# Kernel optimization log

Hardware: AMD Instinct MI355X
Metric: run time of the kernel (lower is better)

The kernel has to match this reference:

```python
import jax, jax.numpy as jnp
import numpy as np

B, N_PER, F_IN, HID, DEG = 64, 1024, 64, 128, 16
N = B * N_PER
E = N * DEG

def _ceil_k(k):
    return -((-4 * k) // 5)  # ceil(0.8 * k), static python int

def setup_inputs():
    key = jax.random.key(0)
    ks = jax.random.split(key, 16)
    x = jax.random.normal(ks[0], (N, F_IN), jnp.float32)
    # edges are intra-graph: local endpoints in [0, N_PER) offset by graph id
    loc = jax.random.randint(ks[1], (2, E), 0, N_PER, jnp.int32)
    gid = jnp.repeat(jnp.arange(B, dtype=jnp.int32), E // B)
    edge_index = loc + gid[None, :] * N_PER
    batch = jnp.repeat(jnp.arange(B, dtype=jnp.int32), N_PER)
    def lin(k, fi, fo):
        s = 1.0 / float(np.sqrt(fi))
        return jax.random.uniform(k, (fi, fo), jnp.float32, -s, s)
    inp = dict(x=x, edge_index=edge_index, batch=batch)
    inp["Wr1"] = lin(ks[2], F_IN, HID); inp["Wn1"] = lin(ks[3], F_IN, HID); inp["b1"] = jnp.zeros((HID,), jnp.float32)
    inp["Wr2"] = lin(ks[4], HID, HID); inp["Wn2"] = lin(ks[5], HID, HID); inp["b2"] = jnp.zeros((HID,), jnp.float32)
    inp["Wr3"] = lin(ks[6], HID, HID); inp["Wn3"] = lin(ks[7], HID, HID); inp["b3"] = jnp.zeros((HID,), jnp.float32)
    inp["p1"] = jax.random.normal(ks[8], (HID,), jnp.float32)
    inp["p2"] = jax.random.normal(ks[9], (HID,), jnp.float32)
    inp["p3"] = jax.random.normal(ks[10], (HID,), jnp.float32)
    inp["l1w"] = lin(ks[11], 2 * HID, HID); inp["l1b"] = jnp.zeros((HID,), jnp.float32)
    inp["l2w"] = lin(ks[12], HID, 2); inp["l2b"] = jnp.zeros((2,), jnp.float32)
    return inp

def _graph_conv(x, src, dst, emask, Wr, Wn, b, n_nodes):
    # x'_i = W1 x_i + sum_{j->i} W2 x_j + b ; masked edges contribute 0
    msg = x[src] * emask[:, None]                                  # [E, H]
    agg = jax.ops.segment_sum(msg, dst, num_segments=n_nodes)     # [N, H]
    return x @ Wr + agg @ Wn + b

def _topk_pool(x, src, dst, emask, p, k_prev):
    # PyG TopKPooling: score = x.p/||p||, keep ceil(0.8*n) per graph,
    # x_out = x[perm] * tanh(score[perm]); relabel+filter edges
    k_new = _ceil_k(k_prev)
    s = (x @ p) / jnp.linalg.norm(p)                               # [B*k_prev]
    vals, idx = jax.lax.top_k(s.reshape(B, k_prev), k_new)        # [B, k_new]
    perm = (idx + jnp.arange(B, dtype=idx.dtype)[:, None] * k_prev).reshape(-1)
    x_new = x[perm] * jnp.tanh(vals.reshape(-1))[:, None]
    inv = jnp.full((B * k_prev,), -1, jnp.int32).at[perm].set(jnp.arange(B * k_new, dtype=jnp.int32))
    ns, nd = inv[src], inv[dst]
    valid = emask * ((ns >= 0) & (nd >= 0)).astype(x.dtype)
    return x_new, jnp.maximum(ns, 0), jnp.maximum(nd, 0), valid, k_new

def _readout(x, k):
    b = jnp.repeat(jnp.arange(B, dtype=jnp.int32), k)
    gmax = jax.ops.segment_max(x, b, num_segments=B)
    gmean = jax.ops.segment_sum(x, b, num_segments=B) / k
    return jnp.concatenate([gmax, gmean], axis=1)                  # [B, 2H]

def reference(x, edge_index, batch, Wr1, Wn1, b1, Wr2, Wn2, b2, Wr3, Wn3, b3, p1, p2, p3, l1w, l1b, l2w, l2b):
    src, dst = edge_index[0], edge_index[1]
    emask = jnp.ones((E,), x.dtype)
    k = N_PER
    convs = [(Wr1, Wn1, b1), (Wr2, Wn2, b2), (Wr3, Wn3, b3)]
    pools = [p1, p2, p3]
    xs = []
    for (Wr, Wn, bb), p in zip(convs, pools):
        x = jax.nn.relu(_graph_conv(x, src, dst, emask, Wr, Wn, bb, B * k))
        x, src, dst, emask, k = _topk_pool(x, src, dst, emask, p, k)
        xs.append(_readout(x, k))
    h = xs[0] + xs[1] + xs[2]
    h = jax.nn.relu(h @ l1w + l1b)
    # F.dropout(p=0.5) skipped: eval-mode reference
    h = jax.nn.relu(h @ l2w + l2b)
    return jax.nn.log_softmax(h, axis=-1)
```

## Files before the change

### kernel.cpp

```cpp
#include <hip/hip_runtime.h>
#include <hip/hip_bf16.h>
#include <math.h>

#define NN   65536
#define NPER 1024
#define NE   1048576
#define NB   64
#define EPG  16384

typedef __attribute__((ext_vector_type(8))) short short8;
typedef __attribute__((ext_vector_type(4))) float f32x4;


__global__ __launch_bounds__(1024) void csr_kernel(const int* __restrict__ ei,
      int* __restrict__ off, int* __restrict__ adj){
  __shared__ int hist[1024];
  __shared__ int wsum[16];
  const int g = ((int)blockIdx.x & 7)*8 + ((int)blockIdx.x >> 3);
  const int t = threadIdx.x;
  const int ebase = g*EPG, nbase = g*NPER;
  hist[t] = 0;
  __syncthreads();
  int srcs[16], dls[16];
  #pragma unroll
  for (int i = 0; i < 16; ++i){
    int e = ebase + t + i*1024;
    srcs[i] = ei[e];
    dls[i]  = ei[NE + e] - nbase;
    atomicAdd(&hist[dls[i]], 1);
  }
  __syncthreads();
  int v = hist[t];
  int lane = t & 63, wid = t >> 6;
  int s = v;
  #pragma unroll
  for (int d = 1; d < 64; d <<= 1){
    int src = (lane >= d) ? (lane - d) : lane;
    int u = __shfl(s, src);
    if (lane >= d) s += u;
  }
  if (lane == 63) wsum[wid] = s;
  __syncthreads();
  if (wid == 0){
    int ws = (lane < 16) ? wsum[lane] : 0;
    #pragma unroll
    for (int d = 1; d < 16; d <<= 1){
      int src = (lane >= d) ? (lane - d) : lane;
      int u = __shfl(ws, src);
      if (lane >= d) ws += u;
    }
    if (lane < 16) wsum[lane] = ws;
  }
  __syncthreads();
  int base = (wid > 0) ? wsum[wid - 1] : 0;
  int excl = base + s - v;
  __syncthreads();
  hist[t] = excl;
  off[nbase + t] = ebase + excl;
  if (g == NB - 1 && t == 1023) off[NN] = NE;
  __syncthreads();
  #pragma unroll
  for (int i = 0; i < 16; ++i){
    int pos = atomicAdd(&hist[dls[i]], 1);
    adj[ebase + pos] = srcs[i];
  }
}


__global__ __launch_bounds__(1024) void gather_kernel(const float* __restrict__ x, int F,
      const int* __restrict__ off, const int* __restrict__ adjB, const float* __restrict__ scl,
      const int* __restrict__ deg2, float* __restrict__ agg, const int* __restrict__ alive){
  int bid = blockIdx.x;
  bid = (bid & 7) * (gridDim.x >> 3) + (bid >> 3);
  int w = bid*16 + ((int)threadIdx.x >> 6);
  int lane = threadIdx.x & 63;
  if (alive && !alive[w]) return;
  int s0 = off[w];
  int s1 = deg2 ? (s0 + deg2[w]) : off[w+1];
  if (F == 64){
    const char* xb = (const char*)x + (lane & 15)*16;
    int sub = lane >> 4;
    float4 a0 = make_float4(0.f,0.f,0.f,0.f), a1 = a0;
    if (s1 > s0){
      for (int e = s0; e < s1; e += 8){
        int e0 = e + sub, e1 = e + 4 + sub;
        bool ok0 = e0 < s1, ok1 = e1 < s1;
        size_t oA = (size_t)(unsigned)adjB[ok0 ? e0 : (s1 - 1)] << 8;
        size_t oB = (size_t)(unsigned)adjB[ok1 ? e1 : (s1 - 1)] << 8;
        float t0 = ok0 ? 1.f : 0.f, t1 = ok1 ? 1.f : 0.f;
        float4 vA = *(const float4*)(xb + oA);
        float4 vB = *(const float4*)(xb + oB);
        a0.x = fmaf(vA.x, t0, a0.x); a0.y = fmaf(vA.y, t0, a0.y);
        a0.z = fmaf(vA.z, t0, a0.z); a0.w = fmaf(vA.w, t0, a0.w);
        a1.x = fmaf(vB.x, t1, a1.x); a1.y = fmaf(vB.y, t1, a1.y);
        a1.z = fmaf(vB.z, t1, a1.z); a1.w = fmaf(vB.w, t1, a1.w);
      }
    }
    a0.x += a1.x; a0.y += a1.y; a0.z += a1.z; a0.w += a1.w;
    #pragma unroll
    for (int m = 16; m <= 32; m <<= 1){
      a0.x += __shfl_xor(a0.x, m);
      a0.y += __shfl_xor(a0.y, m);
      a0.z += __shfl_xor(a0.z, m);
      a0.w += __shfl_xor(a0.w, m);
    }
    if (lane < 16) *(float4*)&agg[(size_t)w*128 + (lane & 15)*4] = a0;
  } else {
    const char* xb = (const char*)x + (lane & 31)*16;
    int sub = lane >> 5;
    float4 a[4];
    #pragma unroll
    for (int i = 0; i < 4; ++i) a[i] = make_float4(0.f,0.f,0.f,0.f);
    if (s1 > s0){
      for (int e = s0; e < s1; e += 8){
        int ss[4]; float tv[4];
        #pragma unroll
        for (int i = 0; i < 4; ++i){
          int ei = e + 2*i + sub;
          bool okE = ei < s1;
          int ii = okE ? ei : (s1 - 1);
          ss[i] = adjB[ii];
          tv[i] = okE ? scl[ii] : 0.f;
        }
        #pragma unroll
        for (int i = 0; i < 4; ++i){
          float4 v = *(const float4*)(xb + (size_t)(unsigned)ss[i]);
          a[i].x = fmaf(v.x, tv[i], a[i].x);
          a[i].y = fmaf(v.y, tv[i], a[i].y);
          a[i].z = fmaf(v.z, tv[i], a[i].z);
          a[i].w = fmaf(v.w, tv[i], a[i].w);
        }
      }
    }
    float4 r;
    r.x = (a[0].x + a[1].x) + (a[2].x + a[3].x);
    r.y = (a[0].y + a[1].y) + (a[2].y + a[3].y);
    r.z = (a[0].z + a[1].z) + (a[2].z + a[3].z);
    r.w = (a[0].w + a[1].w) + (a[2].w + a[3].w);
    r.x += __shfl_xor(r.x, 32);
    r.y += __shfl_xor(r.y, 32);
    r.z += __shfl_xor(r.z, 32);
    r.w += __shfl_xor(r.w, 32);
    if (lane < 32) *(float4*)&agg[(size_t)w*128 + (lane & 31)*4] = r;
  }
}


__global__ __launch_bounds__(256) void wsplit_all_kernel(
      const float* __restrict__ Wr0, const float* __restrict__ Wn0,
      const float* __restrict__ Wr1, const float* __restrict__ Wn1,
      const float* __restrict__ Wr2, const float* __restrict__ Wn2,
      unsigned short* __restrict__ WTh, unsigned short* __restrict__ WTl){
  int idx = blockIdx.x*256 + threadIdx.x;
  int rel, Kcat, Kx, base;
  const float *Wr, *Wn;
  if (idx < 16384){ rel = idx;          Kcat = 128; Kx = 64;  base = 0;     Wr = Wr0; Wn = Wn0; }
  else if (idx < 49152){ rel = idx - 16384; Kcat = 256; Kx = 128; base = 16384; Wr = Wr1; Wn = Wn1; }
  else { rel = idx - 49152; Kcat = 256; Kx = 128; base = 49152; Wr = Wr2; Wn = Wn2; }
  int c = rel & 127, k = rel >> 7;
  float w = (k < Kx) ? Wr[k*128 + c] : Wn[(k - Kx)*128 + c];
  __hip_bfloat16 h = __float2bfloat16(w);
  float hf = __bfloat162float(h);
  __hip_bfloat16 l = __float2bfloat16(w - hf);
  WTh[base + c*Kcat + k] = reinterpret_cast<unsigned short&>(h);
  WTl[base + c*Kcat + k] = reinterpret_cast<unsigned short&>(l);
}


__global__ __launch_bounds__(256, 2) void conv_kernel(const float* __restrict__ xsrc, int strideX, int ntx,
      const float* aggb, int nta,
      const unsigned short* __restrict__ WTh, const unsigned short* __restrict__ WTl, int Kcat,
      const float* __restrict__ bias, const float* __restrict__ p, const float* __restrict__ scaleX,
      float* yout, float* __restrict__ score){
  __shared__ unsigned short XhL[128*32], XlL[128*32];
  __shared__ unsigned short WhL[128*32], WlL[128*32];
  __shared__ float sbuf[128*2];
  const int tid = threadIdx.x;
  const int rblk = ((int)blockIdx.x & 7) * ((int)gridDim.x >> 3) + ((int)blockIdx.x >> 3);
  const int row0 = rblk * 128;
  const int srow = tid & 127;
  const int shalf = tid >> 7;
  const int lane = tid & 63;
  const int wid = tid >> 6;
  const int wr = wid >> 1, wc = wid & 1;
  const int l15 = lane & 15, lkq = lane >> 4;

  const float xscale = scaleX ? scaleX[row0 + srow] : 1.f;

  f32x4 acc[4][4];
  #pragma unroll
  for (int m = 0; m < 4; ++m)
    #pragma unroll
    for (int j = 0; j < 4; ++j)
      acc[m][j] = (f32x4){0.f, 0.f, 0.f, 0.f};

  const int nt = ntx + nta;
  for (int t = 0; t < nt; ++t){
    __syncthreads();
    {
      const float* Xs   = (t < ntx) ? xsrc : aggb;
      const int stride  = (t < ntx) ? strideX : 128;
      const int kc      = (t < ntx) ? t*32 : (t - ntx)*32;
      const float sc    = (t < ntx) ? xscale : 1.f;
      #pragma unroll
      for (int kq2 = 0; kq2 < 2; ++kq2){
        const int kq = shalf*2 + kq2;
        const float* xp = Xs + (size_t)(row0 + srow)*stride + kc + kq*8;
        float4 v0 = *(const float4*)(xp);
        float4 v1 = *(const float4*)(xp + 4);
        float vv[8] = {v0.x*sc, v0.y*sc, v0.z*sc, v0.w*sc,
                       v1.x*sc, v1.y*sc, v1.z*sc, v1.w*sc};
        short8 hs, ls;
        #pragma unroll
        for (int q = 0; q < 8; ++q){
          __hip_bfloat16 h = __float2bfloat16(vv[q]);
          float hf = __bfloat162float(h);
          __hip_bfloat16 lo = __float2bfloat16(vv[q] - hf);
          hs[q] = reinterpret_cast<short&>(h);
          ls[q] = reinterpret_cast<short&>(lo);
        }
        const int kqph = kq ^ (srow & 3);
        *(short8*)&XhL[srow*32 + kqph*8] = hs;
        *(short8*)&XlL[srow*32 + kqph*8] = ls;
      }
      const int kcw = t*32;
      #pragma unroll
      for (int kq2 = 0; kq2 < 2; ++kq2){
        const int kq = shalf*2 + kq2;
        short8 h = *(const short8*)&WTh[(size_t)srow*Kcat + kcw + kq*8];
        short8 l = *(const short8*)&WTl[(size_t)srow*Kcat + kcw + kq*8];
        const int kqph = kq ^ (srow & 3);
        *(short8*)&WhL[srow*32 + kqph*8] = h;
        *(short8*)&WlL[srow*32 + kqph*8] = l;
      }
    }
    __syncthreads();
    short8 bh[4], bl[4];
    #pragma unroll
    for (int j = 0; j < 4; ++j){
      const int col = wc*64 + j*16 + l15;
      const int offb = col*32 + (lkq ^ (col & 3))*8;
      bh[j] = *(const short8*)&WhL[offb];
      bl[j] = *(const short8*)&WlL[offb];
    }
    #pragma unroll
    for (int m = 0; m < 4; ++m){
      const int row = wr*64 + m*16 + l15;
      const int offa = row*32 + (lkq ^ (row & 3))*8;
      short8 ah = *(const short8*)&XhL[offa];
      short8 al = *(const short8*)&XlL[offa];
      #pragma unroll
      for (int j = 0; j < 4; ++j){
        acc[m][j] = __builtin_amdgcn_mfma_f32_16x16x32_bf16(ah, bh[j], acc[m][j], 0, 0, 0);
        acc[m][j] = __builtin_amdgcn_mfma_f32_16x16x32_bf16(ah, bl[j], acc[m][j], 0, 0, 0);
        acc[m][j] = __builtin_amdgcn_mfma_f32_16x16x32_bf16(al, bh[j], acc[m][j], 0, 0, 0);
      }
    }
  }

  #pragma unroll
  for (int m = 0; m < 4; ++m){
    float prt[4] = {0.f, 0.f, 0.f, 0.f};
    #pragma unroll
    for (int j = 0; j < 4; ++j){
      const int col = wc*64 + j*16 + l15;
      const float bcol = bias[col];
      const float pcol = p[col];
      f32x4 a = acc[m][j];
      #pragma unroll
      for (int r = 0; r < 4; ++r){
        const int row = wr*64 + m*16 + lkq*4 + r;
        float y = fmaxf(a[r] + bcol, 0.f);
        yout[(size_t)(row0 + row)*128 + col] = y;
        prt[r] = fmaf(y, pcol, prt[r]);
      }
    }
    #pragma unroll
    for (int r = 0; r < 4; ++r){
      #pragma unroll
      for (int msk = 8; msk >= 1; msk >>= 1) prt[r] += __shfl_xor(prt[r], msk);
      if (l15 == 0) sbuf[(wr*64 + m*16 + lkq*4 + r)*2 + wc] = prt[r];
    }
  }
  __syncthreads();
  if (tid < 128) score[row0 + tid] = sbuf[tid*2] + sbuf[tid*2 + 1];
}


__global__ __launch_bounds__(1024) void topk_kernel(const float* __restrict__ score,
      const int* __restrict__ alive_cur, int* __restrict__ alive_next,
      float* __restrict__ scale, int* __restrict__ selList,
      const float* __restrict__ p, int m){
  __shared__ float lv[1024];
  __shared__ int   li[1024];
  __shared__ float rnorm;
  const int g = ((int)blockIdx.x & 7)*8 + ((int)blockIdx.x >> 3);
  const int t = threadIdx.x;
  if (t < 64){
    float v0 = p[t], v1 = p[t + 64];
    float ss = v0*v0 + v1*v1;
    #pragma unroll
    for (int mm = 32; mm >= 1; mm >>= 1) ss += __shfl_xor(ss, mm);
    if (t == 0) rnorm = rsqrtf(ss);
  }
  const int node = g*NPER + t;
  bool ok = alive_cur ? (alive_cur[node] != 0) : true;
  float v = ok ? score[node] : -INFINITY;
  int idx = node;
  alive_next[node] = 0;
  scale[node] = 0.f;

  auto cex_shfl = [&](int stride, bool dirUp){
    float vj = __shfl_xor(v, stride);
    int   ij = __shfl_xor(idx, stride);
    bool iAmLow = (t & stride) == 0;
    bool mineFirst = (v > vj) || (v == vj && idx < ij);
    bool takeMine = ((dirUp == iAmLow) == mineFirst);
    v   = takeMine ? v   : vj;
    idx = takeMine ? idx : ij;
  };
  auto cex_lds = [&](int stride, bool dirUp){
    __syncthreads();
    lv[t] = v; li[t] = idx;
    __syncthreads();
    float vj = lv[t ^ stride];
    int   ij = li[t ^ stride];
    bool iAmLow = (t & stride) == 0;
    bool mineFirst = (v > vj) || (v == vj && idx < ij);
    bool takeMine = ((dirUp == iAmLow) == mineFirst);
    v   = takeMine ? v   : vj;
    idx = takeMine ? idx : ij;
  };

  #pragma unroll
  for (int size = 2; size <= 64; size <<= 1){
    const bool dirUp = (t & size) == 0;
    for (int stride = size >> 1; stride >= 1; stride >>= 1)
      cex_shfl(stride, dirUp);
  }
  #pragma unroll
  for (int size = 128; size <= 1024; size <<= 1){
    const bool dirUp = (t & size) == 0;
    for (int stride = size >> 1; stride >= 64; stride >>= 1)
      cex_lds(stride, dirUp);
    for (int stride = 32; stride >= 1; stride >>= 1)
      cex_shfl(stride, dirUp);
  }

  if (t < m){
    alive_next[idx] = 1;
    scale[idx] = tanhf(v * rnorm);
    selList[g*NPER + t] = idx;
  }
}


__global__ __launch_bounds__(1024) void readout_kernel(const float* __restrict__ y,
      const float* __restrict__ scale, const int* __restrict__ selList,
      float* __restrict__ h, int m, int firstLevel){
  __shared__ float smx[64][17];
  __shared__ float ssm[64][17];
  int g = ((int)blockIdx.x & 7)*8 + ((int)blockIdx.x >> 3);
  int fq = blockIdx.y;
  int t = threadIdx.x;
  int c  = t >> 4;
  int lf = t & 15;
  int f  = fq*16 + lf;
  const int* sel = selList + g*NPER;
  float mx = -INFINITY, sm = 0.f;
  for (int r = c; r < m; r += 64){
    int node = sel[r];
    float o = y[(size_t)node*128 + f] * scale[node];
    mx = fmaxf(mx, o);
    sm += o;
  }
  smx[c][lf] = mx; ssm[c][lf] = sm;
  __syncthreads();
  for (int s = 32; s > 0; s >>= 1){
    if (c < s){
      smx[c][lf] = fmaxf(smx[c][lf], smx[c+s][lf]);
      ssm[c][lf] += ssm[c+s][lf];
    }
    __syncthreads();
  }
  if (c == 0){
    if (firstLevel){
      h[g*256 + f]       = smx[0][lf];
      h[g*256 + 128 + f] = ssm[0][lf] / (float)m;
    } else {
      h[g*256 + f]       += smx[0][lf];
      h[g*256 + 128 + f] += ssm[0][lf] / (float)m;
    }
  }
}


__global__ __launch_bounds__(1024) void compact_kernel(const int* __restrict__ off, const int* __restrict__ adj,
      const float* __restrict__ scale, const int* __restrict__ alive,
      int* __restrict__ adj2, float* __restrict__ scl2, int* __restrict__ deg2){
  int w = blockIdx.x*16 + ((int)threadIdx.x >> 6);
  int lane = threadIdx.x & 63;
  if (!alive[w]){ if (lane == 0) deg2[w] = 0; return; }
  int s0 = off[w], s1 = off[w+1];
  int base = s0;
  for (int e0 = s0; e0 < s1; e0 += 64){
    int e = e0 + lane;
    bool okE = e < s1;
    int s = adj[okE ? e : (s1 - 1)];
    float t = scale[s];
    bool keep = okE && (t != 0.f);
    unsigned long long m = __ballot(keep);
    int pos = base + __popcll(m & ((1ull << lane) - 1ull));
    if (keep){ adj2[pos] = s << 9; scl2[pos] = t; }
    base += __popcll(m);
  }
  if (lane == 0) deg2[w] = base - s0;
}


__global__ __launch_bounds__(128) void final_kernel(const float* __restrict__ h,
      const float* __restrict__ l1w, const float* __restrict__ l1b,
      const float* __restrict__ l2w, const float* __restrict__ l2b,
      float* __restrict__ out){
  int g = blockIdx.x, t = threadIdx.x;
  __shared__ float hrow[256];
  __shared__ float red0[128], red1[128];
  hrow[t]       = h[g*256 + t];
  hrow[t + 128] = h[g*256 + 128 + t];
  __syncthreads();
  float a = l1b[t];
  for (int k = 0; k < 256; ++k) a = fmaf(hrow[k], l1w[k*128 + t], a);
  a = fmaxf(a, 0.f);
  red0[t] = a * l2w[t*2 + 0];
  red1[t] = a * l2w[t*2 + 1];
  __syncthreads();
  for (int s = 64; s > 0; s >>= 1){
    if (t < s){ red0[t] += red0[t + s]; red1[t] += red1[t + s]; }
    __syncthreads();
  }
  if (t == 0){
    float z0 = fmaxf(red0[0] + l2b[0], 0.f);
    float z1 = fmaxf(red1[0] + l2b[1], 0.f);
    float mz = fmaxf(z0, z1);
    float lse = mz + logf(expf(z0 - mz) + expf(z1 - mz));
    out[g*2 + 0] = z0 - lse;
    out[g*2 + 1] = z1 - lse;
  }
}


static inline size_t alignup(size_t x){ return (x + 255) & ~(size_t)255; }

extern "C" void kernel_launch(void* const* d_in, const int* in_sizes, int n_in,
                              void* d_out, int out_size, void* d_ws, size_t ws_size,
                              hipStream_t stream) {
  const float* x_in = (const float*)d_in[0];
  const int*   ei   = (const int*)d_in[1];
  const float* Wr[3] = {(const float*)d_in[3], (const float*)d_in[6], (const float*)d_in[9]};
  const float* Wn[3] = {(const float*)d_in[4], (const float*)d_in[7], (const float*)d_in[10]};
  const float* bs[3] = {(const float*)d_in[5], (const float*)d_in[8], (const float*)d_in[11]};
  const float* ps[3] = {(const float*)d_in[12], (const float*)d_in[13], (const float*)d_in[14]};
  const float* l1w = (const float*)d_in[15];
  const float* l1b = (const float*)d_in[16];
  const float* l2w = (const float*)d_in[17];
  const float* l2b = (const float*)d_in[18];
  float* out = (float*)d_out;

  char* w = (char*)d_ws;
  size_t o = 0;
  auto take = [&](size_t bytes) -> void* { void* p = w + o; o = alignup(o + bytes); return p; };
  int*   off    = (int*)  take((size_t)(NN + 1) * 4);
  int*   adj    = (int*)  take((size_t)NE * 4);
  int*   adj2   = (int*)  take((size_t)NE * 4);
  float* scl2   = (float*)take((size_t)NE * 4);
  int*   deg2   = (int*)  take((size_t)NN * 4);
  int*   aliveA = (int*)  take((size_t)NN * 4);
  int*   aliveB = (int*)  take((size_t)NN * 4);
  float* scale  = (float*)take((size_t)NN * 4);
  float* score  = (float*)take((size_t)NN * 4);
  int*   selList= (int*)  take((size_t)NN * 4);
  float* h      = (float*)take((size_t)NB * 256 * 4);
  unsigned short* WTh = (unsigned short*)take((size_t)81920 * 2);
  unsigned short* WTl = (unsigned short*)take((size_t)81920 * 2);
  float* A      = (float*)take((size_t)NN * 128 * 4);
  float* Bb     = (float*)take((size_t)NN * 128 * 4);
  (void)ws_size; (void)n_in; (void)in_sizes; (void)out_size;

  csr_kernel<<<NB, 1024, 0, stream>>>(ei, off, adj);
  wsplit_all_kernel<<<320, 256, 0, stream>>>(Wr[0], Wn[0], Wr[1], Wn[1], Wr[2], Wn[2], WTh, WTl);

  const int MS[3]   = {820, 656, 525};
  const int WOFF[3] = {0, 16384, 49152};
  const int KCAT[3] = {128, 256, 256};
  int* aliveCur = nullptr;
  int* aliveNext = aliveA;
  float* bufs[2] = {Bb, A};
  for (int l = 0; l < 3; ++l){
    const int Kx = (l == 0) ? 64 : 128;
    const int Ka = (l == 0) ? 64 : 128;
    float* aggb = bufs[l & 1];
    if (l == 0){
      gather_kernel<<<NN/16, 1024, 0, stream>>>(x_in, 64, off, adj, nullptr, nullptr, aggb, nullptr);
      conv_kernel<<<NN/128, 256, 0, stream>>>(x_in, 64, Kx/32, aggb, Ka/32, WTh + WOFF[0], WTl + WOFF[0], KCAT[0],
                                              bs[0], ps[0], nullptr, aggb, score);
    } else {
      const float* ysrc = bufs[(l - 1) & 1];
      gather_kernel<<<NN/16, 1024, 0, stream>>>(ysrc, 128, off, adj2, scl2, deg2, aggb, aliveCur);
      conv_kernel<<<NN/128, 256, 0, stream>>>(ysrc, 128, Kx/32, aggb, Ka/32, WTh + WOFF[l], WTl + WOFF[l], KCAT[l],
                                              bs[l], ps[l], scale, aggb, score);
    }
    topk_kernel<<<NB, 1024, 0, stream>>>(score, aliveCur, aliveNext, scale, selList, ps[l], MS[l]);
    readout_kernel<<<dim3(NB, 8), 1024, 0, stream>>>(aggb, scale, selList, h, MS[l], (l == 0) ? 1 : 0);
    if (l < 2)
      compact_kernel<<<NN/16, 1024, 0, stream>>>(off, adj, scale, aliveNext, adj2, scl2, deg2);
    aliveCur = aliveNext;
    aliveNext = (l == 0) ? aliveB : aliveA;
  }
  final_kernel<<<NB, 128, 0, stream>>>(h, l1w, l1b, l2w, l2b, out);
}
```

Before: 269.8 us.

## Stage per-graph features in LDS for gather and drop edge compaction pass

Each edge now stores a graph-local source index. The gather kernel is rewritten so each block loads one graph's 16-feature slice, pre-scaled by the pooling scale, into shared memory and sums neighbours from LDS instead of issuing random global loads. This removes the compact kernel and its adjacency/scale buffers, since dropped nodes have zero scale and contribute nothing. In exchange, every edge is traversed again for each of the 4–8 feature slices, and pruned edges are still walked, with 64 KB of LDS per block limiting occupancy.

New measurement: 356.3 us. 1.32x slower.

```diff
diff --git a/kernel.cpp b/kernel.cpp
--- a/kernel.cpp
+++ b/kernel.cpp
@@ -25,7 +25,7 @@
   #pragma unroll
   for (int i = 0; i < 16; ++i){
     int e = ebase + t + i*1024;
-    srcs[i] = ei[e];
+    srcs[i] = ei[e] - nbase;
     dls[i]  = ei[NE + e] - nbase;
     atomicAdd(&hist[dls[i]], 1);
   }
@@ -67,81 +67,52 @@
 }
 
 
-__global__ __launch_bounds__(1024) void gather_kernel(const float* __restrict__ x, int F,
-      const int* __restrict__ off, const int* __restrict__ adjB, const float* __restrict__ scl,
-      const int* __restrict__ deg2, float* __restrict__ agg, const int* __restrict__ alive){
-  int bid = blockIdx.x;
-  bid = (bid & 7) * (gridDim.x >> 3) + (bid >> 3);
-  int w = bid*16 + ((int)threadIdx.x >> 6);
-  int lane = threadIdx.x & 63;
-  if (alive && !alive[w]) return;
-  int s0 = off[w];
-  int s1 = deg2 ? (s0 + deg2[w]) : off[w+1];
-  if (F == 64){
-    const char* xb = (const char*)x + (lane & 15)*16;
-    int sub = lane >> 4;
-    float4 a0 = make_float4(0.f,0.f,0.f,0.f), a1 = a0;
-    if (s1 > s0){
-      for (int e = s0; e < s1; e += 8){
-        int e0 = e + sub, e1 = e + 4 + sub;
-        bool ok0 = e0 < s1, ok1 = e1 < s1;
-        size_t oA = (size_t)(unsigned)adjB[ok0 ? e0 : (s1 - 1)] << 8;
-        size_t oB = (size_t)(unsigned)adjB[ok1 ? e1 : (s1 - 1)] << 8;
-        float t0 = ok0 ? 1.f : 0.f, t1 = ok1 ? 1.f : 0.f;
-        float4 vA = *(const float4*)(xb + oA);
-        float4 vB = *(const float4*)(xb + oB);
-        a0.x = fmaf(vA.x, t0, a0.x); a0.y = fmaf(vA.y, t0, a0.y);
-        a0.z = fmaf(vA.z, t0, a0.z); a0.w = fmaf(vA.w, t0, a0.w);
-        a1.x = fmaf(vB.x, t1, a1.x); a1.y = fmaf(vB.y, t1, a1.y);
-        a1.z = fmaf(vB.z, t1, a1.z); a1.w = fmaf(vB.w, t1, a1.w);
-      }
-    }
-    a0.x += a1.x; a0.y += a1.y; a0.z += a1.z; a0.w += a1.w;
-    #pragma unroll
-    for (int m = 16; m <= 32; m <<= 1){
-      a0.x += __shfl_xor(a0.x, m);
-      a0.y += __shfl_xor(a0.y, m);
-      a0.z += __shfl_xor(a0.z, m);
-      a0.w += __shfl_xor(a0.w, m);
-    }
-    if (lane < 16) *(float4*)&agg[(size_t)w*128 + (lane & 15)*4] = a0;
-  } else {
-    const char* xb = (const char*)x + (lane & 31)*16;
-    int sub = lane >> 5;
-    float4 a[4];
-    #pragma unroll
-    for (int i = 0; i < 4; ++i) a[i] = make_float4(0.f,0.f,0.f,0.f);
-    if (s1 > s0){
-      for (int e = s0; e < s1; e += 8){
-        int ss[4]; float tv[4];
-        #pragma unroll
-        for (int i = 0; i < 4; ++i){
-          int ei = e + 2*i + sub;
-          bool okE = ei < s1;
-          int ii = okE ? ei : (s1 - 1);
-          ss[i] = adjB[ii];
-          tv[i] = okE ? scl[ii] : 0.f;
-        }
-        #pragma unroll
-        for (int i = 0; i < 4; ++i){
-          float4 v = *(const float4*)(xb + (size_t)(unsigned)ss[i]);
-          a[i].x = fmaf(v.x, tv[i], a[i].x);
-          a[i].y = fmaf(v.y, tv[i], a[i].y);
-          a[i].z = fmaf(v.z, tv[i], a[i].z);
-          a[i].w = fmaf(v.w, tv[i], a[i].w);
-        }
-      }
-    }
-    float4 r;
-    r.x = (a[0].x + a[1].x) + (a[2].x + a[3].x);
-    r.y = (a[0].y + a[1].y) + (a[2].y + a[3].y);
-    r.z = (a[0].z + a[1].z) + (a[2].z + a[3].z);
-    r.w = (a[0].w + a[1].w) + (a[2].w + a[3].w);
-    r.x += __shfl_xor(r.x, 32);
-    r.y += __shfl_xor(r.y, 32);
-    r.z += __shfl_xor(r.z, 32);
-    r.w += __shfl_xor(r.w, 32);
-    if (lane < 32) *(float4*)&agg[(size_t)w*128 + (lane & 31)*4] = r;
+__global__ __launch_bounds__(1024) void gatherL_kernel(const float* __restrict__ x, int F,
+      const int* __restrict__ off, const int* __restrict__ adjL,
+      const float* __restrict__ scale, const int* __restrict__ alive,
+      float* __restrict__ agg){
+  __shared__ float yq[1024*16];
+  const int g = ((int)blockIdx.x & 7)*8 + ((int)blockIdx.x >> 3);
+  const int fq = blockIdx.y;
+  const int t = threadIdx.x;
+  const int nbase = g*NPER;
+  {
+    const float sc = scale ? scale[nbase + t] : 1.f;
+    const float* xb = x + (size_t)(nbase + t)*F + fq*16;
+    float4 v0 = *(const float4*)(xb);
+    float4 v1 = *(const float4*)(xb + 4);
+    float4 v2 = *(const float4*)(xb + 8);
+    float4 v3 = *(const float4*)(xb + 12);
+    v0.x *= sc; v0.y *= sc; v0.z *= sc; v0.w *= sc;
+    v1.x *= sc; v1.y *= sc; v1.z *= sc; v1.w *= sc;
+    v2.x *= sc; v2.y *= sc; v2.z *= sc; v2.w *= sc;
+    v3.x *= sc; v3.y *= sc; v3.z *= sc; v3.w *= sc;
+    *(float4*)&yq[t*16 + 0]  = v0;
+    *(float4*)&yq[t*16 + 4]  = v1;
+    *(float4*)&yq[t*16 + 8]  = v2;
+    *(float4*)&yq[t*16 + 12] = v3;
+  }
+  __syncthreads();
+  const int wv = t >> 6, lane = t & 63;
+  const int sub = lane >> 4, fl = lane & 15;
+  for (int n = 0; n < 64; ++n){
+    const int w = nbase + wv*64 + n;
+    if (alive && !alive[w]) continue;
+    const int s0 = off[w], s1 = off[w+1];
+    float a = 0.f;
+    for (int e = s0; e < s1; e += 8){
+      int e0 = e + sub, e1 = e + 4 + sub;
+      bool ok0 = e0 < s1, ok1 = e1 < s1;
+      int src0 = adjL[ok0 ? e0 : (s1 - 1)];
+      int src1 = adjL[ok1 ? e1 : (s1 - 1)];
+      float y0 = yq[src0*16 + fl];
+      float y1 = yq[src1*16 + fl];
+      a += ok0 ? y0 : 0.f;
+      a += ok1 ? y1 : 0.f;
+    }
+    a += __shfl_xor(a, 16);
+    a += __shfl_xor(a, 32);
+    if (lane < 16) agg[(size_t)w*128 + fq*16 + fl] = a;
   }
 }
 
@@ -395,29 +366,6 @@
 }
 
 
-__global__ __launch_bounds__(1024) void compact_kernel(const int* __restrict__ off, const int* __restrict__ adj,
-      const float* __restrict__ scale, const int* __restrict__ alive,
-      int* __restrict__ adj2, float* __restrict__ scl2, int* __restrict__ deg2){
-  int w = blockIdx.x*16 + ((int)threadIdx.x >> 6);
-  int lane = threadIdx.x & 63;
-  if (!alive[w]){ if (lane == 0) deg2[w] = 0; return; }
-  int s0 = off[w], s1 = off[w+1];
-  int base = s0;
-  for (int e0 = s0; e0 < s1; e0 += 64){
-    int e = e0 + lane;
-    bool okE = e < s1;
-    int s = adj[okE ? e : (s1 - 1)];
-    float t = scale[s];
-    bool keep = okE && (t != 0.f);
-    unsigned long long m = __ballot(keep);
-    int pos = base + __popcll(m & ((1ull << lane) - 1ull));
-    if (keep){ adj2[pos] = s << 9; scl2[pos] = t; }
-    base += __popcll(m);
-  }
-  if (lane == 0) deg2[w] = base - s0;
-}
-
-
 __global__ __launch_bounds__(128) void final_kernel(const float* __restrict__ h,
       const float* __restrict__ l1w, const float* __restrict__ l1b,
       const float* __restrict__ l2w, const float* __restrict__ l2b,
@@ -471,9 +419,6 @@
   auto take = [&](size_t bytes) -> void* { void* p = w + o; o = alignup(o + bytes); return p; };
   int*   off    = (int*)  take((size_t)(NN + 1) * 4);
   int*   adj    = (int*)  take((size_t)NE * 4);
-  int*   adj2   = (int*)  take((size_t)NE * 4);
-  float* scl2   = (float*)take((size_t)NE * 4);
-  int*   deg2   = (int*)  take((size_t)NN * 4);
   int*   aliveA = (int*)  take((size_t)NN * 4);
   int*   aliveB = (int*)  take((size_t)NN * 4);
   float* scale  = (float*)take((size_t)NN * 4);
@@ -500,19 +445,17 @@
     const int Ka = (l == 0) ? 64 : 128;
     float* aggb = bufs[l & 1];
     if (l == 0){
-      gather_kernel<<<NN/16, 1024, 0, stream>>>(x_in, 64, off, adj, nullptr, nullptr, aggb, nullptr);
+      gatherL_kernel<<<dim3(NB, 4), 1024, 0, stream>>>(x_in, 64, off, adj, nullptr, nullptr, aggb);
       conv_kernel<<<NN/128, 256, 0, stream>>>(x_in, 64, Kx/32, aggb, Ka/32, WTh + WOFF[0], WTl + WOFF[0], KCAT[0],
                                               bs[0], ps[0], nullptr, aggb, score);
     } else {
       const float* ysrc = bufs[(l - 1) & 1];
-      gather_kernel<<<NN/16, 1024, 0, stream>>>(ysrc, 128, off, adj2, scl2, deg2, aggb, aliveCur);
+      gatherL_kernel<<<dim3(NB, 8), 1024, 0, stream>>>(ysrc, 128, off, adj, scale, aliveCur, aggb);
       conv_kernel<<<NN/128, 256, 0, stream>>>(ysrc, 128, Kx/32, aggb, Ka/32, WTh + WOFF[l], WTl + WOFF[l], KCAT[l],
                                               bs[l], ps[l], scale, aggb, score);
     }
     topk_kernel<<<NB, 1024, 0, stream>>>(score, aliveCur, aliveNext, scale, selList, ps[l], MS[l]);
     readout_kernel<<<dim3(NB, 8), 1024, 0, stream>>>(aggb, scale, selList, h, MS[l], (l == 0) ? 1 : 0);
-    if (l < 2)
-      compact_kernel<<<NN/16, 1024, 0, stream>>>(off, adj, scale, aliveNext, adj2, scl2, deg2);
     aliveCur = aliveNext;
     aliveNext = (l == 0) ? aliveB : aliveA;
   }
```
